# Performance work log

Measured on AMD Instinct MI355X. Metric: run time of the kernel, lower is better.

## Reference

```python
import jax, jax.numpy as jnp
import numpy as np

B, T, E, D, H = 4, 2048, 512, 768, 12
DH = D // H  # 64
S = T + E


def _heads(x, W, b):
    # x: [B, L, D] -> [B, H, L, DH]
    y = x @ W.T + b
    return y.reshape(y.shape[0], y.shape[1], H, DH).transpose(0, 2, 1, 3)


def setup_inputs() -> dict:
    key = jax.random.key(0)
    ks = jax.random.split(key, 16)
    p = lambda k, shape: (jax.random.normal(k, shape, dtype=jnp.float32) * 0.02)
    inp = {
        'token_hidden_states': jax.random.normal(ks[0], (B, T, D), dtype=jnp.float32),
        'entity_hidden_states': jax.random.normal(ks[1], (B, E, D), dtype=jnp.float32),
        'attention_mask': jnp.zeros((B, 1, 1, S), dtype=jnp.float32),
        'query_pos': jax.random.normal(ks[2], (B, E, D), dtype=jnp.float32),
        'Wq': p(ks[3], (D, D)), 'bq': jnp.zeros((D,), jnp.float32),
        'Wk': p(ks[4], (D, D)), 'bk': jnp.zeros((D,), jnp.float32),
        'Wv': p(ks[5], (D, D)), 'bv': jnp.zeros((D,), jnp.float32),
        'Weq': p(ks[6], (D, D)), 'beq': jnp.zeros((D,), jnp.float32),
        'Wek': p(ks[7], (D, D)), 'bek': jnp.zeros((D,), jnp.float32),
        'Wev': p(ks[8], (D, D)), 'bev': jnp.zeros((D,), jnp.float32),
    }
    return inp


def reference(token_hidden_states, entity_hidden_states, attention_mask, query_pos,
              Wq, bq, Wk, bk, Wv, bv, Weq, beq, Wek, bek, Wev, bev):
    pae = (entity_hidden_states + query_pos) * 0.5  # pos-aware entity states
    # Projections into heads: [B, H, L, DH]
    q_w = _heads(token_hidden_states, Wq, bq)
    q_e = _heads(pae, Weq, beq)
    k_w = _heads(token_hidden_states, Wk, bk)
    k_e = _heads(pae, Wek, bek)
    v_w = _heads(token_hidden_states, Wv, bv)
    v_e = _heads(entity_hidden_states, Wev, bev)
    # Concatenating Q and K along the sequence axis reproduces exactly the
    # four-block (w2w, w2e, e2w, e2e) score matrix of the original module.
    q = jnp.concatenate([q_w, q_e], axis=2)  # [B, H, S, DH]
    k = jnp.concatenate([k_w, k_e], axis=2)
    v = jnp.concatenate([v_w, v_e], axis=2)
    scores = jnp.einsum('bhqd,bhkd->bhqk', q, k) / jnp.sqrt(jnp.float32(DH))
    scores = scores + attention_mask  # additive mask, broadcast over heads/queries
    probs = jax.nn.softmax(scores, axis=-1)  # dropout prob = 0 (eval)
    ctx = jnp.einsum('bhqk,bhkd->bhqd', probs, v)  # [B, H, S, DH]
    ctx = ctx.transpose(0, 2, 1, 3).reshape(B, S, D)
    return ctx[:, :T, :], ctx[:, T:, :]
```

## Files before the change

kernel.cpp:

```cpp
#include <hip/hip_runtime.h>
#include <stdint.h>

constexpr int Bn = 4, Tn = 2048, En = 512, Dn = 768, Hn = 12, DHn = 64, Sn = 2560;

typedef __bf16 bf16x8 __attribute__((ext_vector_type(8)));
typedef float f32x4 __attribute__((ext_vector_type(4)));

#define MFMA16x16x32 __builtin_amdgcn_mfma_f32_16x16x32_bf16

#define GLOAD_LDS16(g, l)                                                        \
  __builtin_amdgcn_global_load_lds((const __attribute__((address_space(1))) uint32_t*)(g), \
                                   (__attribute__((address_space(3))) uint32_t*)(l), 16, 0, 0)

#define QSCALE 0.1803368843f
#define LOG2E  1.4426950409f

__device__ __forceinline__ unsigned short f2bf(float f) {
  union { float f; uint32_t u; } c;
  c.f = f;
  return (unsigned short)((c.u + 0x7fffu + ((c.u >> 16) & 1u)) >> 16);
}

__global__ __launch_bounds__(256) void prep_all(
    const float* __restrict__ tok, const float* __restrict__ ent,
    const float* __restrict__ qp, const float* __restrict__ mask,
    const float* __restrict__ w0, const float* __restrict__ w1, const float* __restrict__ w2,
    const float* __restrict__ w3, const float* __restrict__ w4, const float* __restrict__ w5,
    unsigned short* __restrict__ Xw, unsigned short* __restrict__ Xq,
    unsigned short* __restrict__ Xe, unsigned short* __restrict__ Wc,
    float* __restrict__ maskS)
{
  const int TOK4 = Bn * Tn * Dn / 4;
  const int ENT4 = Bn * En * Dn / 4;
  const int W4 = Dn * Dn / 4;
  int i = blockIdx.x * 256 + threadIdx.x;
  if (i < TOK4) {
    float4 v = ((const float4*)tok)[i];
    ushort4 o = { f2bf(v.x), f2bf(v.y), f2bf(v.z), f2bf(v.w) };
    ((ushort4*)Xw)[i] = o;
    return;
  }
  i -= TOK4;
  if (i < ENT4) {
    float4 e = ((const float4*)ent)[i];
    float4 q = ((const float4*)qp)[i];
    ushort4 p = { f2bf((e.x + q.x) * 0.5f), f2bf((e.y + q.y) * 0.5f),
                  f2bf((e.z + q.z) * 0.5f), f2bf((e.w + q.w) * 0.5f) };
    ushort4 x = { f2bf(e.x), f2bf(e.y), f2bf(e.z), f2bf(e.w) };
    ((ushort4*)Xq)[i] = p;
    ((ushort4*)Xe)[i] = x;
    return;
  }
  i -= ENT4;
  if (i < 6 * W4) {
    int wi = i / W4, off = i - wi * W4;
    const float* src = (wi == 0) ? w0 : (wi == 1) ? w1 : (wi == 2) ? w2
                     : (wi == 3) ? w3 : (wi == 4) ? w4 : w5;
    float4 v = ((const float4*)src)[off];
    ushort4 o = { f2bf(v.x), f2bf(v.y), f2bf(v.z), f2bf(v.w) };
    ((ushort4*)Wc)[i] = o;
    return;
  }
  i -= 6 * W4;
  {
    float4 v = ((const float4*)mask)[i];
    float4 o = { v.x * LOG2E, v.y * LOG2E, v.z * LOG2E, v.w * LOG2E };
    ((float4*)maskS)[i] = o;
  }
}

__global__ __launch_bounds__(256, 2) void proj_gemm(
    const unsigned short* __restrict__ Xw_, const unsigned short* __restrict__ Xq_,
    const unsigned short* __restrict__ Xe_, const unsigned short* __restrict__ Wc,
    const float* __restrict__ b0, const float* __restrict__ b1, const float* __restrict__ b2,
    const float* __restrict__ b3, const float* __restrict__ b4, const float* __restrict__ b5,
    unsigned short* __restrict__ Qb, unsigned short* __restrict__ Kb, unsigned short* __restrict__ Vtb)
{
  const int z = blockIdx.z;
  const bool tokseg = (blockIdx.x < 64);
  const int m0 = tokseg ? blockIdx.x * 128 : (blockIdx.x - 64) * 128;
  const int widx = tokseg ? z : z + 3;
  const unsigned short* X = tokseg ? Xw_ : ((z == 2) ? Xe_ : Xq_);
  const unsigned short* W = Wc + (size_t)widx * Dn * Dn;
  const float* bias = (widx == 0) ? b0 : (widx == 1) ? b1 : (widx == 2) ? b2
                    : (widx == 3) ? b3 : (widx == 4) ? b4 : b5;
  const bool swap = (z != 2);
  const float oscale = (z == 0) ? QSCALE : 1.0f;
  const int batch = tokseg ? (m0 >> 11) : (m0 >> 9);
  const int sbase = tokseg ? (m0 & 2047) : (Tn + (m0 & 511));

  const int t = threadIdx.x;
  const int lane = t & 63, wave = t >> 6;
  const int l15 = lane & 15, g = lane >> 4;
  const int n0 = blockIdx.y * 128;

  __shared__ __align__(16) unsigned short ldsX[2][4096];
  __shared__ __align__(16) unsigned short ldsW[2][4096];

  f32x4 acc[4][4];
#pragma unroll
  for (int a = 0; a < 4; ++a)
#pragma unroll
    for (int b = 0; b < 4; ++b) acc[a][b] = (f32x4){0.f, 0.f, 0.f, 0.f};

  auto stage = [&](int buf, int k0) {
#pragma unroll
    for (int i = 0; i < 2; ++i) {
      int idx0 = i * 256 + wave * 64;
      int r = (idx0 + lane) >> 2;
      int ko = k0 + ((lane & 3) << 3);
      GLOAD_LDS16(X + (size_t)(m0 + r) * Dn + ko, &ldsX[buf][idx0 * 8]);
      GLOAD_LDS16(W + (size_t)(n0 + r) * Dn + ko, &ldsW[buf][idx0 * 8]);
    }
  };

  stage(0, 0);
  __syncthreads();

  const int aw = wave >> 1, bw = wave & 1;

  for (int ks = 0; ks < 24; ++ks) {
    int cur = ks & 1;
    if (ks < 23) stage(cur ^ 1, (ks + 1) * 32);
    const unsigned short* tX = ldsX[cur];
    const unsigned short* tW = ldsW[cur];
    const unsigned short* tA = swap ? tW : tX;
    const unsigned short* tB = swap ? tX : tW;
    bf16x8 af[4], bfr[4];
#pragma unroll
    for (int f = 0; f < 4; ++f) {
      int r = aw * 64 + f * 16 + l15;
      af[f] = *(const bf16x8*)(tA + r * 32 + (g << 3));
    }
#pragma unroll
    for (int f = 0; f < 4; ++f) {
      int r = bw * 64 + f * 16 + l15;
      bfr[f] = *(const bf16x8*)(tB + r * 32 + (g << 3));
    }
    __builtin_amdgcn_s_setprio(1);
#pragma unroll
    for (int mf = 0; mf < 4; ++mf)
#pragma unroll
      for (int nf = 0; nf < 4; ++nf)
        acc[mf][nf] = MFMA16x16x32(af[mf], bfr[nf], acc[mf][nf], 0, 0, 0);
    __builtin_amdgcn_s_setprio(0);
    __syncthreads();
  }

  if (swap) {
    unsigned short* outb = (z == 0) ? Qb : Kb;
#pragma unroll
    for (int mf = 0; mf < 4; ++mf) {
      int n = n0 + aw * 64 + mf * 16 + 4 * g;
      float4 b4 = *(const float4*)(bias + n);
      int h = n >> 6, dh0 = n & 63;
#pragma unroll
      for (int nf = 0; nf < 4; ++nf) {
        int s = sbase + bw * 64 + nf * 16 + l15;
        f32x4 a = acc[mf][nf];
        ushort4 o = { f2bf((a[0] + b4.x) * oscale), f2bf((a[1] + b4.y) * oscale),
                      f2bf((a[2] + b4.z) * oscale), f2bf((a[3] + b4.w) * oscale) };
        *(ushort4*)(outb + (((size_t)batch * Hn + h) * Sn + s) * DHn + dh0) = o;
      }
    }
  } else {
#pragma unroll
    for (int nf = 0; nf < 4; ++nf) {
      int n = n0 + bw * 64 + nf * 16 + l15;
      float bv = bias[n];
      int h = n >> 6, dh = n & 63;
      size_t vtrow = ((size_t)batch * Hn + h) * DHn + dh;
#pragma unroll
      for (int mf = 0; mf < 4; ++mf) {
        int s = sbase + aw * 64 + mf * 16 + 4 * g;
        f32x4 a = acc[mf][nf];
        ushort4 o = { f2bf(a[0] + bv), f2bf(a[1] + bv), f2bf(a[2] + bv), f2bf(a[3] + bv) };
        *(ushort4*)(Vtb + vtrow * Sn + s) = o;
      }
    }
  }
}

__global__ __launch_bounds__(256, 4) void attn_kernel(
    const unsigned short* __restrict__ Qb, const unsigned short* __restrict__ Kb,
    const unsigned short* __restrict__ Vtb, const float* __restrict__ maskS,
    float* __restrict__ out)
{
  const int t = threadIdx.x, lane = t & 63, wave = t >> 6;
  const int l15 = lane & 15, g = lane >> 4;

  const int bid = blockIdx.y * 20 + blockIdx.x;
  const int swz = (bid & 7) * 120 + (bid >> 3);
  const int bx = swz % 20, by = swz / 20;
  const int bb = by / Hn, h = by % Hn;
  const int qw = bx * 128 + wave * 32;

  __shared__ __align__(16) unsigned short Klds[2][4096];
  __shared__ __align__(16) unsigned short Vlds[2][4096];

  const size_t headQ = ((size_t)bb * Hn + h) * Sn * DHn;
  const size_t headV = ((size_t)bb * Hn + h) * DHn * Sn;

  auto stage = [&](int buf, int c) {
    const int kv0 = c * 64;
#pragma unroll
    for (int i = 0; i < 2; ++i) {
      int idx0 = i * 256 + wave * 64;
      int r = (idx0 + lane) >> 3;
      int ssl = ((lane & 7) ^ (r & 7)) << 3;
      GLOAD_LDS16(Kb + headQ + (size_t)(kv0 + r) * DHn + ssl, &Klds[buf][idx0 * 8]);
      GLOAD_LDS16(Vtb + headV + (size_t)r * Sn + kv0 + ssl, &Vlds[buf][idx0 * 8]);
    }
  };

  bf16x8 qf[2][2];
#pragma unroll
  for (int i = 0; i < 2; ++i)
#pragma unroll
    for (int kq = 0; kq < 2; ++kq)
      qf[i][kq] = *(const bf16x8*)(Qb + headQ + (size_t)(qw + i * 16 + l15) * DHn + kq * 32 + g * 8);

  const int l7 = l15 & 7;
  int koff[2], voff[2][2];
#pragma unroll
  for (int kq = 0; kq < 2; ++kq)
    koff[kq] = l15 * 128 + (((kq * 4 + g) ^ l7) << 4);
#pragma unroll
  for (int ksv = 0; ksv < 2; ++ksv)
#pragma unroll
    for (int hf = 0; hf < 2; ++hf)
      voff[ksv][hf] = l15 * 128 + (((4 * ksv + 2 * hf + (g >> 1)) ^ l7) << 4) + (g & 1) * 8;

  bf16x8 ones;
#pragma unroll
  for (int j = 0; j < 8; ++j) ones[j] = (l15 == 0) ? (__bf16)1.0f : (__bf16)0.0f;

  f32x4 ctx[2][4];
  f32x4 ctxl[2];
#pragma unroll
  for (int i = 0; i < 2; ++i) {
#pragma unroll
    for (int d = 0; d < 4; ++d) ctx[i][d] = (f32x4){0.f, 0.f, 0.f, 0.f};
    ctxl[i] = (f32x4){0.f, 0.f, 0.f, 0.f};
  }

  const char* KBp = (const char*)Klds;
  const char* VBp = (const char*)Vlds;
  const float* maskB = maskS + (size_t)bb * Sn;

  auto compute = [&](const int buf, const int c) {
    const int kv0 = c * 64;
    const char* KB = KBp + buf * 8192;
    const char* VB = VBp + buf * 8192;

    f32x4 mvv[4];
#pragma unroll
    for (int kvf = 0; kvf < 4; ++kvf) {
      float4 mv = *(const float4*)(maskB + kv0 + kvf * 16 + g * 4);
      mvv[kvf] = (f32x4){mv.x, mv.y, mv.z, mv.w};
    }

    f32x4 sacc[2][4];
#pragma unroll
    for (int kvf = 0; kvf < 4; ++kvf) {
      bf16x8 kf0 = *(const bf16x8*)(KB + kvf * 2048 + koff[0]);
      bf16x8 kf1 = *(const bf16x8*)(KB + kvf * 2048 + koff[1]);
      __builtin_amdgcn_s_setprio(1);
      f32x4 s0 = MFMA16x16x32(kf0, qf[0][0], mvv[kvf], 0, 0, 0);
      sacc[0][kvf] = MFMA16x16x32(kf1, qf[0][1], s0, 0, 0, 0);
      f32x4 s1 = MFMA16x16x32(kf0, qf[1][0], mvv[kvf], 0, 0, 0);
      sacc[1][kvf] = MFMA16x16x32(kf1, qf[1][1], s1, 0, 0, 0);
      __builtin_amdgcn_s_setprio(0);
    }

    bf16x8 pb[2][2];
#pragma unroll
    for (int i = 0; i < 2; ++i)
#pragma unroll
      for (int ksv = 0; ksv < 2; ++ksv)
#pragma unroll
        for (int r = 0; r < 4; ++r) {
          pb[i][ksv][r]     = (__bf16)__builtin_amdgcn_exp2f(sacc[i][2 * ksv][r]);
          pb[i][ksv][4 + r] = (__bf16)__builtin_amdgcn_exp2f(sacc[i][2 * ksv + 1][r]);
        }

#pragma unroll
    for (int ksv = 0; ksv < 2; ++ksv) {
#pragma unroll
      for (int df = 0; df < 4; ++df) {
        union { uint64_t u[2]; bf16x8 v; } vv;
        vv.u[0] = *(const uint64_t*)(VB + df * 2048 + voff[ksv][0]);
        vv.u[1] = *(const uint64_t*)(VB + df * 2048 + voff[ksv][1]);
        __builtin_amdgcn_s_setprio(1);
        ctx[0][df] = MFMA16x16x32(vv.v, pb[0][ksv], ctx[0][df], 0, 0, 0);
        ctx[1][df] = MFMA16x16x32(vv.v, pb[1][ksv], ctx[1][df], 0, 0, 0);
        __builtin_amdgcn_s_setprio(0);
      }
      ctxl[0] = MFMA16x16x32(ones, pb[0][ksv], ctxl[0], 0, 0, 0);
      ctxl[1] = MFMA16x16x32(ones, pb[1][ksv], ctxl[1], 0, 0, 0);
    }
  };

  stage(0, 0);

  for (int c = 0; c < Sn / 64; c += 2) {
    __syncthreads();
    stage(1, c + 1);
    compute(0, c);
    __syncthreads();
    if (c + 2 < Sn / 64) stage(0, c + 2);
    compute(1, c + 1);
  }

#pragma unroll
  for (int i = 0; i < 2; ++i) {
    float lsum = __shfl(ctxl[i][0], l15);
    float inv = 1.0f / lsum;
    int q = qw + i * 16 + l15;
    size_t rowoff;
    if (q < Tn) rowoff = ((size_t)bb * Tn + q) * Dn;
    else        rowoff = (size_t)Bn * Tn * Dn + ((size_t)bb * En + (q - Tn)) * Dn;
#pragma unroll
    for (int df = 0; df < 4; ++df) {
      int d = h * DHn + df * 16 + 4 * g;
      float4 o = { ctx[i][df][0] * inv, ctx[i][df][1] * inv, ctx[i][df][2] * inv, ctx[i][df][3] * inv };
      *(float4*)(out + rowoff + d) = o;
    }
  }
}

extern "C" void kernel_launch(void* const* d_in, const int* in_sizes, int n_in,
                              void* d_out, int out_size, void* d_ws, size_t ws_size,
                              hipStream_t stream) {
  (void)in_sizes; (void)n_in; (void)out_size; (void)ws_size;
  const float* tok  = (const float*)d_in[0];
  const float* ent  = (const float*)d_in[1];
  const float* mask = (const float*)d_in[2];
  const float* qpos = (const float*)d_in[3];
  const float* Wq = (const float*)d_in[4];  const float* bq = (const float*)d_in[5];
  const float* Wk = (const float*)d_in[6];  const float* bk = (const float*)d_in[7];
  const float* Wv = (const float*)d_in[8];  const float* bv = (const float*)d_in[9];
  const float* Weq = (const float*)d_in[10]; const float* beq = (const float*)d_in[11];
  const float* Wek = (const float*)d_in[12]; const float* bek = (const float*)d_in[13];
  const float* Wev = (const float*)d_in[14]; const float* bev = (const float*)d_in[15];
  float* out = (float*)d_out;

  unsigned short* ws = (unsigned short*)d_ws;
  const size_t headN = (size_t)Bn * Hn * Sn * DHn;
  unsigned short* Qb  = ws;
  unsigned short* Kb  = Qb + headN;
  unsigned short* Vtb = Kb + headN;
  unsigned short* Xw  = Vtb + headN;
  unsigned short* Xq  = Xw + (size_t)Bn * Tn * Dn;
  unsigned short* Xe  = Xq + (size_t)Bn * En * Dn;
  unsigned short* Wc  = Xe + (size_t)Bn * En * Dn;
  float* maskS = (float*)(Wc + 6 * (size_t)Dn * Dn);

  const int TOK4 = Bn * Tn * Dn / 4;
  const int ENT4 = Bn * En * Dn / 4;
  const int W4 = Dn * Dn / 4;
  const int MSK4 = Bn * Sn / 4;
  const int total4 = TOK4 + ENT4 + 6 * W4 + MSK4;
  prep_all<<<dim3((total4 + 255) / 256), 256, 0, stream>>>(
      tok, ent, qpos, mask, Wq, Wk, Wv, Weq, Wek, Wev, Xw, Xq, Xe, Wc, maskS);

  proj_gemm<<<dim3(80, Dn / 128, 3), 256, 0, stream>>>(
      Xw, Xq, Xe, Wc, bq, bk, bv, beq, bek, bev, Qb, Kb, Vtb);

  attn_kernel<<<dim3(Sn / 128, Bn * Hn), 256, 0, stream>>>(Qb, Kb, Vtb, maskS, out);
}
```

Baseline: 162.0 us.

## Split attention KV range across two blocks and add a combine kernel

The attention kernel gets a template split factor. With a split of two, each query tile's KV sequence is processed by two blocks, doubling the grid. Each half writes unnormalized context and row sums: the first half into the output buffer, the second into a workspace buffer. A new combine kernel then adds the two halves and divides by the summed row totals. The aim is more parallelism and better CU load balance, at the cost of an extra pass over the full fp32 output, more workspace, and a dependence on the workspace being large enough.

```diff
diff --git a/kernel.cpp b/kernel.cpp
--- a/kernel.cpp
+++ b/kernel.cpp
@@ -181,19 +181,26 @@
   }
 }
 
+template<int NSPLIT>
 __global__ __launch_bounds__(256, 4) void attn_kernel(
     const unsigned short* __restrict__ Qb, const unsigned short* __restrict__ Kb,
     const unsigned short* __restrict__ Vtb, const float* __restrict__ maskS,
-    float* __restrict__ out)
+    float* __restrict__ out, float* __restrict__ ctxP, float* __restrict__ Lbuf)
 {
   const int t = threadIdx.x, lane = t & 63, wave = t >> 6;
   const int l15 = lane & 15, g = lane >> 4;
 
-  const int bid = blockIdx.y * 20 + blockIdx.x;
-  const int swz = (bid & 7) * 120 + (bid >> 3);
-  const int bx = swz % 20, by = swz / 20;
+  const int nx = 20 * NSPLIT;
+  const int bid = blockIdx.y * nx + blockIdx.x;
+  const int perx = (48 * nx) >> 3;
+  const int swz = (bid & 7) * perx + (bid >> 3);
+  const int bx = swz % nx, by = swz / nx;
   const int bb = by / Hn, h = by % Hn;
-  const int qw = bx * 128 + wave * 32;
+  const int qt = (NSPLIT == 2) ? (bx >> 1) : bx;
+  const int half = (NSPLIT == 2) ? (bx & 1) : 0;
+  const int qw = qt * 128 + wave * 32;
+  const int kvbase = half * (Sn / NSPLIT);
+  const int nchunk = Sn / 64 / NSPLIT;
 
   __shared__ __align__(16) unsigned short Klds[2][4096];
   __shared__ __align__(16) unsigned short Vlds[2][4096];
@@ -202,7 +209,7 @@
   const size_t headV = ((size_t)bb * Hn + h) * DHn * Sn;
 
   auto stage = [&](int buf, int c) {
-    const int kv0 = c * 64;
+    const int kv0 = kvbase + c * 64;
 #pragma unroll
     for (int i = 0; i < 2; ++i) {
       int idx0 = i * 256 + wave * 64;
@@ -249,7 +256,7 @@
   const float* maskB = maskS + (size_t)bb * Sn;
 
   auto compute = [&](const int buf, const int c) {
-    const int kv0 = c * 64;
+    const int kv0 = kvbase + c * 64;
     const char* KB = KBp + buf * 8192;
     const char* VB = VBp + buf * 8192;
 
@@ -303,36 +310,71 @@
 
   stage(0, 0);
 
-  for (int c = 0; c < Sn / 64; c += 2) {
+  for (int c = 0; c < nchunk; c += 2) {
     __syncthreads();
     stage(1, c + 1);
     compute(0, c);
     __syncthreads();
-    if (c + 2 < Sn / 64) stage(0, c + 2);
+    if (c + 2 < nchunk) stage(0, c + 2);
     compute(1, c + 1);
   }
 
 #pragma unroll
   for (int i = 0; i < 2; ++i) {
     float lsum = __shfl(ctxl[i][0], l15);
-    float inv = 1.0f / lsum;
     int q = qw + i * 16 + l15;
     size_t rowoff;
     if (q < Tn) rowoff = ((size_t)bb * Tn + q) * Dn;
     else        rowoff = (size_t)Bn * Tn * Dn + ((size_t)bb * En + (q - Tn)) * Dn;
-#pragma unroll
-    for (int df = 0; df < 4; ++df) {
-      int d = h * DHn + df * 16 + 4 * g;
-      float4 o = { ctx[i][df][0] * inv, ctx[i][df][1] * inv, ctx[i][df][2] * inv, ctx[i][df][3] * inv };
-      *(float4*)(out + rowoff + d) = o;
-    }
+    if (NSPLIT == 1) {
+      float inv = 1.0f / lsum;
+#pragma unroll
+      for (int df = 0; df < 4; ++df) {
+        int d = h * DHn + df * 16 + 4 * g;
+        float4 o = { ctx[i][df][0] * inv, ctx[i][df][1] * inv, ctx[i][df][2] * inv, ctx[i][df][3] * inv };
+        *(float4*)(out + rowoff + d) = o;
+      }
+    } else {
+      if (g == 0)
+        Lbuf[(size_t)half * (Bn * Hn * Sn) + ((size_t)bb * Hn + h) * Sn + q] = lsum;
+      float* obase = half ? ctxP : out;
+#pragma unroll
+      for (int df = 0; df < 4; ++df) {
+        int d = h * DHn + df * 16 + 4 * g;
+        float4 o = { ctx[i][df][0], ctx[i][df][1], ctx[i][df][2], ctx[i][df][3] };
+        *(float4*)(obase + rowoff + d) = o;
+      }
+    }
+  }
+}
+
+__global__ __launch_bounds__(256) void combine_kernel(
+    float* __restrict__ out, const float* __restrict__ ctxP, const float* __restrict__ Lbuf)
+{
+  const int N4 = Bn * Sn * Dn / 4;
+  const int BTD4 = Bn * Tn * Dn / 4;
+  const int L1off = Bn * Hn * Sn;
+  for (int idx = blockIdx.x * 256 + threadIdx.x; idx < N4; idx += gridDim.x * 256) {
+    int r = idx / 192;
+    int d4 = idx - r * 192;
+    int hh = d4 >> 4;
+    int b, q;
+    if (idx < BTD4) { b = r >> 11; q = r & 2047; }
+    else { int r2 = r - Bn * Tn; b = r2 >> 9; q = Tn + (r2 & 511); }
+    int li = (b * Hn + hh) * Sn + q;
+    float inv = 1.0f / (Lbuf[li] + Lbuf[L1off + li]);
+    float4 o = ((const float4*)out)[idx];
+    float4 p = ((const float4*)ctxP)[idx];
+    float4 res = { (o.x + p.x) * inv, (o.y + p.y) * inv,
+                   (o.z + p.z) * inv, (o.w + p.w) * inv };
+    ((float4*)out)[idx] = res;
   }
 }
 
 extern "C" void kernel_launch(void* const* d_in, const int* in_sizes, int n_in,
                               void* d_out, int out_size, void* d_ws, size_t ws_size,
                               hipStream_t stream) {
-  (void)in_sizes; (void)n_in; (void)out_size; (void)ws_size;
+  (void)in_sizes; (void)n_in; (void)out_size;
   const float* tok  = (const float*)d_in[0];
   const float* ent  = (const float*)d_in[1];
   const float* mask = (const float*)d_in[2];
@@ -354,7 +396,19 @@
   unsigned short* Xq  = Xw + (size_t)Bn * Tn * Dn;
   unsigned short* Xe  = Xq + (size_t)Bn * En * Dn;
   unsigned short* Wc  = Xe + (size_t)Bn * En * Dn;
-  float* maskS = (float*)(Wc + 6 * (size_t)Dn * Dn);
+
+  const size_t ctxPoff  = (size_t)3 * headN * 2;
+  const size_t ctxPsz   = (size_t)Bn * Hn * Sn * DHn * 4;
+  const size_t lbufoff  = ctxPoff + ctxPsz;
+  const size_t lbufsz   = (size_t)2 * Bn * Hn * Sn * 4;
+  const size_t masksoff = lbufoff + lbufsz;
+  const size_t NEED_SPLIT = masksoff + (size_t)Bn * Sn * 4;
+  const bool split = (ws_size >= NEED_SPLIT);
+
+  float* ctxP = (float*)((char*)d_ws + ctxPoff);
+  float* Lbuf = (float*)((char*)d_ws + lbufoff);
+  float* maskS = split ? (float*)((char*)d_ws + masksoff)
+                       : (float*)(Wc + 6 * (size_t)Dn * Dn);
 
   const int TOK4 = Bn * Tn * Dn / 4;
   const int ENT4 = Bn * En * Dn / 4;
@@ -367,5 +421,10 @@
   proj_gemm<<<dim3(80, Dn / 128, 3), 256, 0, stream>>>(
       Xw, Xq, Xe, Wc, bq, bk, bv, beq, bek, bev, Qb, Kb, Vtb);
 
-  attn_kernel<<<dim3(Sn / 128, Bn * Hn), 256, 0, stream>>>(Qb, Kb, Vtb, maskS, out);
-}
+  if (split) {
+    attn_kernel<2><<<dim3(40, Bn * Hn), 256, 0, stream>>>(Qb, Kb, Vtb, maskS, out, ctxP, Lbuf);
+    combine_kernel<<<dim3(2048), 256, 0, stream>>>(out, ctxP, Lbuf);
+  } else {
+    attn_kernel<1><<<dim3(20, Bn * Hn), 256, 0, stream>>>(Qb, Kb, Vtb, maskS, out, ctxP, Lbuf);
+  }
+}
```

Result: slower. 179.6 us (+10.9%).

## Pre-swizzle V into MFMA fragment layout and load it directly from global

Applied to the files above, without the earlier changes.

The projection GEMM now writes V in a layout matching the per-lane MFMA B-operand fragments, so the attention kernel reads each V fragment with one 16-byte global load per lane and no longer stages V through LDS. The row-sum is accumulated in registers from the exp values and reduced with cross-lane shuffles, replacing the extra MFMA against a ones vector. Launch bounds drop from 4 to 3 blocks per CU to make room for the extra V registers. This removes LDS traffic and MFMA work for V and the sum, at the cost of non-overlapped global loads for V, which are shared across the 20 query blocks of each head, and lower occupancy.

```diff
diff --git a/kernel.cpp b/kernel.cpp
--- a/kernel.cpp
+++ b/kernel.cpp
@@ -74,7 +74,7 @@
     const unsigned short* __restrict__ Xe_, const unsigned short* __restrict__ Wc,
     const float* __restrict__ b0, const float* __restrict__ b1, const float* __restrict__ b2,
     const float* __restrict__ b3, const float* __restrict__ b4, const float* __restrict__ b5,
-    unsigned short* __restrict__ Qb, unsigned short* __restrict__ Kb, unsigned short* __restrict__ Vtb)
+    unsigned short* __restrict__ Qb, unsigned short* __restrict__ Kb, unsigned short* __restrict__ Vsb)
 {
   const int z = blockIdx.z;
   const bool tokseg = (blockIdx.x < 64);
@@ -169,21 +169,25 @@
       int n = n0 + bw * 64 + nf * 16 + l15;
       float bv = bias[n];
       int h = n >> 6, dh = n & 63;
-      size_t vtrow = ((size_t)batch * Hn + h) * DHn + dh;
+      int df = (dh >> 4) & 3;
+      size_t headO = ((size_t)batch * Hn + h) * Sn * DHn;
 #pragma unroll
       for (int mf = 0; mf < 4; ++mf) {
         int s = sbase + aw * 64 + mf * 16 + 4 * g;
+        int c = s >> 6, ksv = (s >> 5) & 1, hi = (s >> 4) & 1;
         f32x4 a = acc[mf][nf];
         ushort4 o = { f2bf(a[0] + bv), f2bf(a[1] + bv), f2bf(a[2] + bv), f2bf(a[3] + bv) };
-        *(ushort4*)(Vtb + vtrow * Sn + s) = o;
+        size_t off = headO + (size_t)c * 4096 + (size_t)((ksv * 4 + df) * 512)
+                   + (size_t)((g * 16 + l15) * 8) + hi * 4;
+        *(ushort4*)(Vsb + off) = o;
       }
     }
   }
 }
 
-__global__ __launch_bounds__(256, 4) void attn_kernel(
+__global__ __launch_bounds__(256, 3) void attn_kernel(
     const unsigned short* __restrict__ Qb, const unsigned short* __restrict__ Kb,
-    const unsigned short* __restrict__ Vtb, const float* __restrict__ maskS,
+    const unsigned short* __restrict__ Vsb, const float* __restrict__ maskS,
     float* __restrict__ out)
 {
   const int t = threadIdx.x, lane = t & 63, wave = t >> 6;
@@ -196,10 +200,8 @@
   const int qw = bx * 128 + wave * 32;
 
   __shared__ __align__(16) unsigned short Klds[2][4096];
-  __shared__ __align__(16) unsigned short Vlds[2][4096];
-
-  const size_t headQ = ((size_t)bb * Hn + h) * Sn * DHn;
-  const size_t headV = ((size_t)bb * Hn + h) * DHn * Sn;
+
+  const size_t headOff = ((size_t)bb * Hn + h) * Sn * DHn;
 
   auto stage = [&](int buf, int c) {
     const int kv0 = c * 64;
@@ -208,8 +210,7 @@
       int idx0 = i * 256 + wave * 64;
       int r = (idx0 + lane) >> 3;
       int ssl = ((lane & 7) ^ (r & 7)) << 3;
-      GLOAD_LDS16(Kb + headQ + (size_t)(kv0 + r) * DHn + ssl, &Klds[buf][idx0 * 8]);
-      GLOAD_LDS16(Vtb + headV + (size_t)r * Sn + kv0 + ssl, &Vlds[buf][idx0 * 8]);
+      GLOAD_LDS16(Kb + headOff + (size_t)(kv0 + r) * DHn + ssl, &Klds[buf][idx0 * 8]);
     }
   };
 
@@ -218,86 +219,80 @@
   for (int i = 0; i < 2; ++i)
 #pragma unroll
     for (int kq = 0; kq < 2; ++kq)
-      qf[i][kq] = *(const bf16x8*)(Qb + headQ + (size_t)(qw + i * 16 + l15) * DHn + kq * 32 + g * 8);
+      qf[i][kq] = *(const bf16x8*)(Qb + headOff + (size_t)(qw + i * 16 + l15) * DHn + kq * 32 + g * 8);
 
   const int l7 = l15 & 7;
-  int koff[2], voff[2][2];
+  int koff[2];
 #pragma unroll
   for (int kq = 0; kq < 2; ++kq)
     koff[kq] = l15 * 128 + (((kq * 4 + g) ^ l7) << 4);
-#pragma unroll
-  for (int ksv = 0; ksv < 2; ++ksv)
-#pragma unroll
-    for (int hf = 0; hf < 2; ++hf)
-      voff[ksv][hf] = l15 * 128 + (((4 * ksv + 2 * hf + (g >> 1)) ^ l7) << 4) + (g & 1) * 8;
-
-  bf16x8 ones;
-#pragma unroll
-  for (int j = 0; j < 8; ++j) ones[j] = (l15 == 0) ? (__bf16)1.0f : (__bf16)0.0f;
+
+  const unsigned short* vlane = Vsb + headOff + lane * 8;
 
   f32x4 ctx[2][4];
-  f32x4 ctxl[2];
+  float lacc[2];
 #pragma unroll
   for (int i = 0; i < 2; ++i) {
 #pragma unroll
     for (int d = 0; d < 4; ++d) ctx[i][d] = (f32x4){0.f, 0.f, 0.f, 0.f};
-    ctxl[i] = (f32x4){0.f, 0.f, 0.f, 0.f};
+    lacc[i] = 0.f;
   }
 
   const char* KBp = (const char*)Klds;
-  const char* VBp = (const char*)Vlds;
   const float* maskB = maskS + (size_t)bb * Sn;
 
   auto compute = [&](const int buf, const int c) {
     const int kv0 = c * 64;
     const char* KB = KBp + buf * 8192;
-    const char* VB = VBp + buf * 8192;
-
-    f32x4 mvv[4];
+
+    bf16x8 vf[2][4];
+#pragma unroll
+    for (int ksv = 0; ksv < 2; ++ksv)
+#pragma unroll
+      for (int df = 0; df < 4; ++df)
+        vf[ksv][df] = *(const bf16x8*)(vlane + (size_t)c * 4096 + (ksv * 4 + df) * 512);
+
+    f32x4 sacc[2][4];
 #pragma unroll
     for (int kvf = 0; kvf < 4; ++kvf) {
       float4 mv = *(const float4*)(maskB + kv0 + kvf * 16 + g * 4);
-      mvv[kvf] = (f32x4){mv.x, mv.y, mv.z, mv.w};
-    }
-
-    f32x4 sacc[2][4];
-#pragma unroll
-    for (int kvf = 0; kvf < 4; ++kvf) {
+      f32x4 mvv = (f32x4){mv.x, mv.y, mv.z, mv.w};
       bf16x8 kf0 = *(const bf16x8*)(KB + kvf * 2048 + koff[0]);
       bf16x8 kf1 = *(const bf16x8*)(KB + kvf * 2048 + koff[1]);
       __builtin_amdgcn_s_setprio(1);
-      f32x4 s0 = MFMA16x16x32(kf0, qf[0][0], mvv[kvf], 0, 0, 0);
+      f32x4 s0 = MFMA16x16x32(kf0, qf[0][0], mvv, 0, 0, 0);
       sacc[0][kvf] = MFMA16x16x32(kf1, qf[0][1], s0, 0, 0, 0);
-      f32x4 s1 = MFMA16x16x32(kf0, qf[1][0], mvv[kvf], 0, 0, 0);
+      f32x4 s1 = MFMA16x16x32(kf0, qf[1][0], mvv, 0, 0, 0);
       sacc[1][kvf] = MFMA16x16x32(kf1, qf[1][1], s1, 0, 0, 0);
       __builtin_amdgcn_s_setprio(0);
     }
 
     bf16x8 pb[2][2];
 #pragma unroll
-    for (int i = 0; i < 2; ++i)
+    for (int i = 0; i < 2; ++i) {
+      float ls = 0.f;
 #pragma unroll
       for (int ksv = 0; ksv < 2; ++ksv)
 #pragma unroll
         for (int r = 0; r < 4; ++r) {
-          pb[i][ksv][r]     = (__bf16)__builtin_amdgcn_exp2f(sacc[i][2 * ksv][r]);
-          pb[i][ksv][4 + r] = (__bf16)__builtin_amdgcn_exp2f(sacc[i][2 * ksv + 1][r]);
+          float e0 = __builtin_amdgcn_exp2f(sacc[i][2 * ksv][r]);
+          float e1 = __builtin_amdgcn_exp2f(sacc[i][2 * ksv + 1][r]);
+          pb[i][ksv][r]     = (__bf16)e0;
+          pb[i][ksv][4 + r] = (__bf16)e1;
+          ls += e0 + e1;
         }
+      lacc[i] += ls;
+    }
 
 #pragma unroll
     for (int ksv = 0; ksv < 2; ++ksv) {
 #pragma unroll
       for (int df = 0; df < 4; ++df) {
-        union { uint64_t u[2]; bf16x8 v; } vv;
-        vv.u[0] = *(const uint64_t*)(VB + df * 2048 + voff[ksv][0]);
-        vv.u[1] = *(const uint64_t*)(VB + df * 2048 + voff[ksv][1]);
         __builtin_amdgcn_s_setprio(1);
-        ctx[0][df] = MFMA16x16x32(vv.v, pb[0][ksv], ctx[0][df], 0, 0, 0);
-        ctx[1][df] = MFMA16x16x32(vv.v, pb[1][ksv], ctx[1][df], 0, 0, 0);
+        ctx[0][df] = MFMA16x16x32(vf[ksv][df], pb[0][ksv], ctx[0][df], 0, 0, 0);
+        ctx[1][df] = MFMA16x16x32(vf[ksv][df], pb[1][ksv], ctx[1][df], 0, 0, 0);
         __builtin_amdgcn_s_setprio(0);
       }
-      ctxl[0] = MFMA16x16x32(ones, pb[0][ksv], ctxl[0], 0, 0, 0);
-      ctxl[1] = MFMA16x16x32(ones, pb[1][ksv], ctxl[1], 0, 0, 0);
     }
   };
 
@@ -314,7 +309,9 @@
 
 #pragma unroll
   for (int i = 0; i < 2; ++i) {
-    float lsum = __shfl(ctxl[i][0], l15);
+    float lsum = lacc[i];
+    lsum += __shfl_xor(lsum, 16);
+    lsum += __shfl_xor(lsum, 32);
     float inv = 1.0f / lsum;
     int q = qw + i * 16 + l15;
     size_t rowoff;
@@ -349,8 +346,8 @@
   const size_t headN = (size_t)Bn * Hn * Sn * DHn;
   unsigned short* Qb  = ws;
   unsigned short* Kb  = Qb + headN;
-  unsigned short* Vtb = Kb + headN;
-  unsigned short* Xw  = Vtb + headN;
+  unsigned short* Vsb = Kb + headN;
+  unsigned short* Xw  = Vsb + headN;
   unsigned short* Xq  = Xw + (size_t)Bn * Tn * Dn;
   unsigned short* Xe  = Xq + (size_t)Bn * En * Dn;
   unsigned short* Wc  = Xe + (size_t)Bn * En * Dn;
@@ -365,7 +362,7 @@
       tok, ent, qpos, mask, Wq, Wk, Wv, Weq, Wek, Wev, Xw, Xq, Xe, Wc, maskS);
 
   proj_gemm<<<dim3(80, Dn / 128, 3), 256, 0, stream>>>(
-      Xw, Xq, Xe, Wc, bq, bk, bv, beq, bek, bev, Qb, Kb, Vtb);
-
-  attn_kernel<<<dim3(Sn / 128, Bn * Hn), 256, 0, stream>>>(Qb, Kb, Vtb, maskS, out);
-}
+      Xw, Xq, Xe, Wc, bq, bk, bv, beq, bek, bev, Qb, Kb, Vsb);
+
+  attn_kernel<<<dim3(Sn / 128, Bn * Hn), 256, 0, stream>>>(Qb, Kb, Vsb, maskS, out);
+}
```

Measured after the change: 198.6 us. +22.6%, slower.
